# Performance work log

Hardware: AMD Instinct MI355X
Metric: run time of the kernel (lower is better)

Reference implementation:

```python
import jax, jax.numpy as jnp
import numpy as np

IFZ = 256      # in_features
SFZ = 1280     # sequence_features
AHZ = 8        # attention heads
AFZ = 64       # attention feature dim per head
NRES = 20      # canonical_num_residues
SCALE = float(np.sqrt(AFZ))
RESID = float(np.sqrt(2.0))
EPS = 1e-6


def _ln(x, s, b, eps=1e-5):
    m = jnp.mean(x, axis=-1, keepdims=True)
    v = jnp.var(x, axis=-1, keepdims=True)
    return (x - m) / jnp.sqrt(v + eps) * s + b


def setup_inputs() -> dict:
    key = jax.random.key(0)
    ks = jax.random.split(key, 20)
    N, B, S = 4096, 4, 512
    HD = AHZ * AFZ
    w = lambda k, shp: (jax.random.normal(k, shp, jnp.float32) * 0.02)
    d = {}
    d["x"] = jax.random.normal(ks[0], (N, IFZ), jnp.float32)
    d["packed_sequence_emb"] = jax.random.normal(ks[1], (B, S, SFZ), jnp.float32)
    d["packed_sequence_mask"] = jnp.ones((B, S), jnp.float32)
    d["prot_mask"] = jnp.arange(N, dtype=jnp.int32)
    d["batch"] = jax.random.randint(ks[2], (N,), 0, B, jnp.int32)
    # projections (bias=False)
    d["Wq"] = w(ks[3], (HD, IFZ))
    d["Wk"] = w(ks[4], (HD, SFZ))
    d["Wv"] = w(ks[5], (HD, SFZ))
    # ag: LayerNorm(HD) -> Linear(HD, IFZ, bias=False) (dropout = identity at eval)
    d["ag_ln_s"] = jnp.ones((HD,), jnp.float32)
    d["ag_ln_b"] = jnp.zeros((HD,), jnp.float32)
    d["Wag"] = w(ks[6], (IFZ, HD))
    d["res_ln_s"] = jnp.ones((3, IFZ), jnp.float32)
    d["res_ln_b"] = jnp.zeros((3, IFZ), jnp.float32)
    d["res_w1"] = w(ks[7], (3, IFZ, IFZ))
    d["res_b1"] = jnp.zeros((3, IFZ), jnp.float32)
    d["res_w2"] = w(ks[8], (3, IFZ, IFZ))
    d["res_b2"] = jnp.zeros((3, IFZ), jnp.float32)
    d["head_w"] = w(ks[9], (NRES, IFZ))
    d["head_b"] = jnp.zeros((NRES,), jnp.float32)
    # output LayerNorm en
    d["en_s"] = jnp.ones((IFZ,), jnp.float32)
    d["en_b"] = jnp.zeros((IFZ,), jnp.float32)
    return d


def _forward(x, emb, mask, prot_mask, batch, Wq, Wk, Wv, ag_ln_s, ag_ln_b, Wag,
             res_ln_s, res_ln_b, res_w1, res_b1, res_w2, res_b2,
             head_w, head_b, en_s, en_b):
    N = x.shape[0]
    B, S = emb.shape[:2]
    b_idx = batch[prot_mask]                      # [M]
    xp = x[prot_mask]                             # [M, IFZ]
    M = xp.shape[0]
    q = (xp @ Wq.T).reshape(M, AHZ, AFZ)          # [M,H,D]
    k = (emb @ Wk.T).reshape(B, S, AHZ, AFZ)      # [B,S,H,D]
    v = (emb @ Wv.T).reshape(B, S, AHZ, AFZ)
    # score vs every protein, then pick own protein (avoids materializing [M,S,H,D] gather)
    scores_all = jnp.einsum('mhd,bshd->mbsh', q, k) / SCALE          # [M,B,S,H]
    sel = b_idx[:, None, None, None]
    scores = jnp.take_along_axis(scores_all, sel, axis=1)[:, 0]       # [M,S,H]
    mb = mask[b_idx][:, :, None]                                      # [M,S,1]
    # padded_sequence_softmax: softmax over S, zero pads, renormalize
    sm = jax.nn.softmax(scores, axis=1) * mb
    w = sm / (jnp.sum(sm, axis=1, keepdims=True) + EPS)               # [M,S,H]
    feat_all = jnp.einsum('msh,bshd->mbhd', w, v)                     # [M,B,H,D]
    feat = jnp.take_along_axis(feat_all, sel, axis=1)[:, 0]
    feat = feat.reshape(M, AHZ * AFZ)
    ag = _ln(feat, ag_ln_s, ag_ln_b) @ Wag.T                          # [M, IFZ]
    # seq_aa_head on the scattered new features (identical to ag for unique prot_mask)
    h = ag
    for i in range(3):
        y = _ln(h, res_ln_s[i], res_ln_b[i])
        y = jax.nn.relu(y @ res_w1[i].T + res_b1[i])
        y = y @ res_w2[i].T + res_b2[i]
        h = (h + y) / RESID
    logits = h @ head_w.T + head_b                                     # [M, NRES]
    new_features = jnp.zeros_like(x).at[prot_mask].set(ag)
    seq_aa_logits = jnp.zeros((N, NRES), x.dtype).at[prot_mask].set(logits)
    unpacked_scores = jnp.zeros((N, S, AHZ), x.dtype).at[prot_mask].set(scores)
    out_x = _ln(x + new_features / RESID, en_s, en_b)
    return out_x, seq_aa_logits, unpacked_scores


def reference(x, packed_sequence_emb, packed_sequence_mask, prot_mask, batch,
              Wq, Wk, Wv, ag_ln_s, ag_ln_b, Wag,
              res_ln_s, res_ln_b, res_w1, res_b1, res_w2, res_b2,
              head_w, head_b, en_s, en_b):
    return _forward(x, packed_sequence_emb, packed_sequence_mask, prot_mask, batch,
                    Wq, Wk, Wv, ag_ln_s, ag_ln_b, Wag,
                    res_ln_s, res_ln_b, res_w1, res_b1, res_w2, res_b2,
                    head_w, head_b, en_s, en_b)
```

## Files before the change

kernel.cpp:

```cpp
#include <hip/hip_runtime.h>
#include <math.h>


typedef short bf8 __attribute__((ext_vector_type(8)));
typedef short bf4 __attribute__((ext_vector_type(4)));
typedef float f32x4 __attribute__((ext_vector_type(4)));
typedef unsigned short u16;

constexpr int LDT = 40;
#define RSQRT2 0.70710678118654752f

__device__ __forceinline__ u16 f2bf(float f) {
  unsigned int u = __builtin_bit_cast(unsigned int, f);
  unsigned int r = u + 0x7fffu + ((u >> 16) & 1u);
  return (u16)(r >> 16);
}
__device__ __forceinline__ float bf2f(u16 v) {
  return __builtin_bit_cast(float, (unsigned int)v << 16);
}
__device__ __forceinline__ f32x4 mfma16(bf8 a, bf8 b, f32x4 c) {
  return __builtin_amdgcn_mfma_f32_16x16x32_bf16(a, b, c, 0, 0, 0);
}

struct CvtDesc { const float* src; u16* dst; int n; };
struct CvtArgs { CvtDesc d[8]; int blk0[9]; };

__global__ __launch_bounds__(256) void cvt_k(
    CvtArgs a, const int* __restrict__ pm, const int* __restrict__ batch,
    int* __restrict__ list, int* __restrict__ inv, int* __restrict__ cnt,
    int N) {
  const int blk = blockIdx.x;
  if (blk >= a.blk0[8]) {
    int m = (blk - a.blk0[8]) * 256 + threadIdx.x;
    if (m >= N) return;
    int p = pm[m];
    int b = batch[p];
    int slot = atomicAdd(&cnt[b], 1);
    list[(size_t)b * N + slot] = m;
    inv[p] = m;
    return;
  }
  int d = 0;
#pragma unroll
  for (int k = 1; k < 8; ++k)
    if (blk >= a.blk0[k]) d = k;
  CvtDesc dd = a.d[d];
  int i = ((blk - a.blk0[d]) * 256 + threadIdx.x) * 8;
  if (i >= dd.n) return;
  f32x4 v0 = *(const f32x4*)(dd.src + i);
  f32x4 v1 = *(const f32x4*)(dd.src + i + 4);
  bf8 o;
  o[0] = (short)f2bf(v0[0]); o[1] = (short)f2bf(v0[1]);
  o[2] = (short)f2bf(v0[2]); o[3] = (short)f2bf(v0[3]);
  o[4] = (short)f2bf(v1[0]); o[5] = (short)f2bf(v1[1]);
  o[6] = (short)f2bf(v1[2]); o[7] = (short)f2bf(v1[3]);
  *(bf8*)(dd.dst + i) = o;
}

__global__ void init_idx_k(int* __restrict__ list, int* __restrict__ inv,
                           int* __restrict__ cnt, int N, int B) {
  int i = blockIdx.x * 256 + threadIdx.x;
  if (i < B * N) list[i] = -1;
  if (i < N) inv[i] = -1;
  if (i < B) cnt[i] = 0;
}

__device__ __forceinline__ void proj64_body(
    u16 (*As)[64 * LDT], u16 (*Bs)[64 * LDT],
    const u16* __restrict__ A, const u16* __restrict__ B,
    u16* __restrict__ C, int M, int Nn, int K, int lda, int ldb, int ldc,
    const int* __restrict__ gatherA, int m0, int n0, u16* __restrict__ VTout) {
  const int tid = threadIdx.x;
  const int wave = tid >> 6, lane = tid & 63;
  const int wm = (wave & 1) * 32, wn = (wave >> 1) * 32;
  const int lrow = lane & 15, quad = lane >> 4;
  const int srow = tid >> 2, skq = tid & 3;
  const bf8 z8 = {0, 0, 0, 0, 0, 0, 0, 0};
  const int off = srow * LDT + skq * 8;

  int gr0 = m0 + srow;
  int ar0 = (gr0 < M) ? (gatherA ? gatherA[gr0] : gr0) : -1;
  const u16* Ap0 = (ar0 >= 0) ? A + (size_t)ar0 * lda + skq * 8 : nullptr;
  const u16* Bp = (n0 + srow < Nn) ? B + (size_t)(n0 + srow) * ldb + skq * 8 : nullptr;

  {
    bf8 a0 = Ap0 ? *(const bf8*)Ap0 : z8;
    bf8 bv = Bp ? *(const bf8*)Bp : z8;
    *(bf8*)&As[0][off] = a0;
    *(bf8*)&Bs[0][off] = bv;
  }
  __syncthreads();

  f32x4 acc[2][2];
#pragma unroll
  for (int i = 0; i < 2; ++i)
#pragma unroll
    for (int j = 0; j < 2; ++j) acc[i][j] = (f32x4){0.f, 0.f, 0.f, 0.f};

  int cur = 0;
  for (int k0 = 0; k0 < K; k0 += 32) {
    const bool more = (k0 + 32 < K);
    bf8 na, nb;
    if (more) {
      na = Ap0 ? *(const bf8*)(Ap0 + k0 + 32) : z8;
      nb = Bp ? *(const bf8*)(Bp + k0 + 32) : z8;
    }
    bf8 af0 = *(const bf8*)&As[cur][(wm + lrow) * LDT + quad * 8];
    bf8 af1 = *(const bf8*)&As[cur][(wm + 16 + lrow) * LDT + quad * 8];
    bf8 bf0 = *(const bf8*)&Bs[cur][(wn + lrow) * LDT + quad * 8];
    bf8 bf1 = *(const bf8*)&Bs[cur][(wn + 16 + lrow) * LDT + quad * 8];
    acc[0][0] = mfma16(af0, bf0, acc[0][0]);
    acc[0][1] = mfma16(af0, bf1, acc[0][1]);
    acc[1][0] = mfma16(af1, bf0, acc[1][0]);
    acc[1][1] = mfma16(af1, bf1, acc[1][1]);
    if (more) {
      *(bf8*)&As[cur ^ 1][off] = na;
      *(bf8*)&Bs[cur ^ 1][off] = nb;
    }
    __syncthreads();
    cur ^= 1;
  }

#pragma unroll
  for (int i = 0; i < 2; ++i) {
    const int row0 = m0 + wm + i * 16 + quad * 4;
#pragma unroll
    for (int j = 0; j < 2; ++j) {
      int col = n0 + wn + j * 16 + lrow;
      if (col >= Nn) continue;
      if (VTout && col >= 512) {
        if (row0 < M) {
          int b = row0 >> 9, sl = row0 & 511;
          bf4 o;
#pragma unroll
          for (int r = 0; r < 4; ++r) o[r] = (short)f2bf(acc[i][j][r]);
          *(bf4*)&VTout[((size_t)(b * 512 + (col - 512)) * 512) + sl] = o;
        }
        continue;
      }
#pragma unroll
      for (int r = 0; r < 4; ++r) {
        int row = row0 + r;
        if (row >= M) continue;
        if (gatherA && gatherA[row] < 0) continue;
        C[(size_t)row * ldc + col] = f2bf(acc[i][j][r]);
      }
    }
  }
}

__global__ __launch_bounds__(256) void qkvproj_k(
    const u16* __restrict__ embbf, const u16* __restrict__ Wkvbf,
    u16* __restrict__ KVbf, u16* __restrict__ VT,
    const u16* __restrict__ xbf, const u16* __restrict__ Wqbf,
    u16* __restrict__ Qbf, const int* __restrict__ pm,
    int MKV, int N, int nkv) {
  __shared__ __align__(16) u16 As[2][64 * LDT];
  __shared__ __align__(16) u16 Bs[2][64 * LDT];
  const int blk = blockIdx.x;
  if (blk < nkv) {
    int by = blk >> 4, bx = blk & 15;
    proj64_body(As, Bs, embbf, Wkvbf, KVbf, MKV, 1024, 1280, 1280, 1280, 1024,
                nullptr, by * 64, bx * 64, VT);
  } else {
    int t = blk - nkv;
    int by = t >> 3, bx = t & 7;
    proj64_body(As, Bs, xbf, Wqbf, Qbf, N, 512, 256, 256, 256, 512,
                pm, by * 64, bx * 64, nullptr);
  }
}

constexpr int WST = 520;
constexpr int QST = 72;

__global__ __launch_bounds__(256) void attn_fused(
    const u16* __restrict__ Q, const u16* __restrict__ KV,
    const u16* __restrict__ VT, const int* __restrict__ list,
    const float* __restrict__ mask, u16* __restrict__ packed,
    u16* __restrict__ feat, int N) {
  const int NMT = gridDim.x;
  const int lin = blockIdx.y * NMT + blockIdx.x;
  const int xcd = lin & 7, rest = lin >> 3;
  const int mt = rest % NMT;
  const int y = ((rest / NMT) << 3) | xcd;
  const int b = y >> 3, h = y & 7;
  const int* lst = list + (size_t)b * N + mt * 32;
  if (lst[0] < 0) return;

  __shared__ __align__(16) u16 Ws[32 * WST];
  __shared__ __align__(16) u16 Qs[32 * QST];
  __shared__ __align__(16) u16 KVs[64 * QST];
  __shared__ __align__(16) float mk[8][68];
  __shared__ int mS[32];

  const int tid = threadIdx.x;
  const int wave = tid >> 6, lane = tid & 63;
  const int wm = (wave & 1) * 16, wns = (wave >> 1) * 32;
  const int lrow = lane & 15, quad = lane >> 4;
  const bf8 z8 = {0, 0, 0, 0, 0, 0, 0, 0};

  const int c0 = tid * 2, c1 = tid * 2 + 1;
  const int sr0 = c0 >> 3, kq0 = c0 & 7;
  const int sr1 = c1 >> 3, kq1 = c1 & 7;
  u16* kvw0 = &KVs[sr0 * QST + kq0 * 8];
  u16* kvw1 = &KVs[sr1 * QST + kq1 * 8];

  if (tid < 32) mS[tid] = lst[tid];
  {
    int p = tid >> 5, j = (tid & 31) * 2;
    *(float2*)&mk[p][j] = *(const float2*)&mask[(size_t)b * 512 + p * 64 + j];
  }
  {
    int qr = tid >> 3, kq = tid & 7;
    int m = lst[qr];
    *(bf8*)&Qs[qr * QST + kq * 8] =
        (m >= 0) ? *(const bf8*)(Q + (size_t)m * 512 + h * 64 + kq * 8) : z8;
  }
  const u16* KVb = KV + (size_t)(b * 512) * 1024 + h * 64;
  {
    int sta = mt & 7;
    *(bf8*)kvw0 = *(const bf8*)(KVb + (size_t)(sta * 64 + sr0) * 1024 + kq0 * 8);
    *(bf8*)kvw1 = *(const bf8*)(KVb + (size_t)(sta * 64 + sr1) * 1024 + kq1 * 8);
  }
  __syncthreads();

  const bf8 qa0 = *(const bf8*)&Qs[(wm + lrow) * QST + 0 + quad * 8];
  const bf8 qa1 = *(const bf8*)&Qs[(wm + lrow) * QST + 32 + quad * 8];

  bf8 r0, r1;
  for (int st = 0; st < 8; ++st) {
    const int sta = (st + mt) & 7;
    if (st < 7) {
      int nx = (st + 1 + mt) & 7;
      r0 = *(const bf8*)(KVb + (size_t)(nx * 64 + sr0) * 1024 + kq0 * 8);
      r1 = *(const bf8*)(KVb + (size_t)(nx * 64 + sr1) * 1024 + kq1 * 8);
    }
    f32x4 acc0 = {0.f, 0.f, 0.f, 0.f}, acc1 = acc0;
    {
      bf8 b00 = *(const bf8*)&KVs[(wns + lrow) * QST + quad * 8];
      bf8 b10 = *(const bf8*)&KVs[(wns + 16 + lrow) * QST + quad * 8];
      bf8 b01 = *(const bf8*)&KVs[(wns + lrow) * QST + 32 + quad * 8];
      bf8 b11 = *(const bf8*)&KVs[(wns + 16 + lrow) * QST + 32 + quad * 8];
      __builtin_amdgcn_s_setprio(1);
      acc0 = mfma16(qa0, b00, acc0);
      acc1 = mfma16(qa0, b10, acc1);
      acc0 = mfma16(qa1, b01, acc0);
      acc1 = mfma16(qa1, b11, acc1);
      __builtin_amdgcn_s_setprio(0);
    }
#pragma unroll
    for (int r = 0; r < 4; ++r) {
      int lr = wm + quad * 4 + r;
      Ws[lr * WST + sta * 64 + wns + lrow] = f2bf(acc0[r] * 0.125f);
      Ws[lr * WST + sta * 64 + wns + 16 + lrow] = f2bf(acc1[r] * 0.125f);
    }
    __syncthreads();
    if (st < 7) {
      *(bf8*)kvw0 = r0;
      *(bf8*)kvw1 = r1;
      __syncthreads();
    }
  }

  const u16* VTb = VT + (size_t)(b * 512 + h * 64) * 512;
  bf8 v0p = *(const bf8*)(VTb + (size_t)sr0 * 512 + ((mt & 7) << 6) + kq0 * 8);
  bf8 v1p = *(const bf8*)(VTb + (size_t)sr1 * 512 + ((mt & 7) << 6) + kq1 * 8);

  {
    const int row = tid >> 3, part = tid & 7;
    u16* wrow = &Ws[row * WST + part * 64];
    const int mm = mS[row];
    bf8 w[8];
    float mx = -1e30f;
#pragma unroll
    for (int v = 0; v < 8; ++v) {
      w[v] = *(const bf8*)(wrow + v * 8);
#pragma unroll
      for (int j = 0; j < 8; ++j) mx = fmaxf(mx, bf2f((u16)w[v][j]));
    }
    if (mm >= 0) {
      u16* prow = packed + ((size_t)h * N + mm) * 512 + part * 64;
#pragma unroll
      for (int v = 0; v < 8; ++v) *(bf8*)(prow + v * 8) = w[v];
    }
#pragma unroll
    for (int d = 1; d < 8; d <<= 1) mx = fmaxf(mx, __shfl_xor(mx, d));
    float ev[64];
    float se = 0.f, ms = 0.f;
#pragma unroll
    for (int v = 0; v < 8; ++v) {
      f32x4 m0 = *(const f32x4*)&mk[part][v * 8];
      f32x4 m1 = *(const f32x4*)&mk[part][v * 8 + 4];
#pragma unroll
      for (int j = 0; j < 8; ++j) {
        float e = __expf(bf2f((u16)w[v][j]) - mx);
        ev[v * 8 + j] = e;
        se += e;
        ms += e * (j < 4 ? m0[j] : m1[j - 4]);
      }
    }
#pragma unroll
    for (int d = 1; d < 8; d <<= 1) {
      se += __shfl_xor(se, d);
      ms += __shfl_xor(ms, d);
    }
    float iv = 1.0f / (ms + 1e-6f * se);
#pragma unroll
    for (int v = 0; v < 8; ++v) {
      f32x4 m0 = *(const f32x4*)&mk[part][v * 8];
      f32x4 m1 = *(const f32x4*)&mk[part][v * 8 + 4];
      bf8 o;
#pragma unroll
      for (int j = 0; j < 8; ++j)
        o[j] = (short)f2bf(ev[v * 8 + j] * (j < 4 ? m0[j] : m1[j - 4]) * iv);
      *(bf8*)(wrow + v * 8) = o;
    }
  }
  __syncthreads();
  *(bf8*)kvw0 = v0p;
  *(bf8*)kvw1 = v1p;
  __syncthreads();

  f32x4 acc0 = {0.f, 0.f, 0.f, 0.f}, acc1 = acc0;
  for (int ss = 0; ss < 8; ++ss) {
    const int s0 = ((ss + mt) & 7) << 6;
    if (ss < 7) {
      int nx = ((ss + 1 + mt) & 7) << 6;
      v0p = *(const bf8*)(VTb + (size_t)sr0 * 512 + nx + kq0 * 8);
      v1p = *(const bf8*)(VTb + (size_t)sr1 * 512 + nx + kq1 * 8);
    }
#pragma unroll
    for (int k0 = 0; k0 < 64; k0 += 32) {
      bf8 a = *(const bf8*)&Ws[(wm + lrow) * WST + s0 + k0 + quad * 8];
      bf8 b0 = *(const bf8*)&KVs[(wns + lrow) * QST + k0 + quad * 8];
      bf8 b1 = *(const bf8*)&KVs[(wns + 16 + lrow) * QST + k0 + quad * 8];
      __builtin_amdgcn_s_setprio(1);
      acc0 = mfma16(a, b0, acc0);
      acc1 = mfma16(a, b1, acc1);
      __builtin_amdgcn_s_setprio(0);
    }
    __syncthreads();
    if (ss < 7) {
      *(bf8*)kvw0 = v0p;
      *(bf8*)kvw1 = v1p;
      __syncthreads();
    }
  }
#pragma unroll
  for (int r = 0; r < 4; ++r) {
    int lr = wm + quad * 4 + r;
    int mm = mS[lr];
    if (mm < 0) continue;
    u16* frow = feat + (size_t)mm * 512 + h * 64;
    frow[wns + lrow] = f2bf(acc0[r]);
    frow[wns + 16 + lrow] = f2bf(acc1[r]);
  }
}

constexpr int HST = 268;
constexpr int AST = 520;
constexpr int YST = 280;
constexpr int SMEM_BYTES = 16 * HST * 4 + 16 * AST * 2 + 16 * YST * 2;

__global__ __launch_bounds__(1024) void mlp_unpack(
    const u16* __restrict__ feat, const float* __restrict__ ag_s,
    const float* __restrict__ ag_b, const u16* __restrict__ Wag,
    const float* __restrict__ x, const float* __restrict__ ens,
    const float* __restrict__ enb, const float* __restrict__ rls,
    const float* __restrict__ rlb, const u16* __restrict__ rw1,
    const float* __restrict__ rb1, const u16* __restrict__ rw2,
    const float* __restrict__ rb2, const float* __restrict__ hw,
    const float* __restrict__ hb, const int* __restrict__ pm,
    const u16* __restrict__ packed, float* __restrict__ out_sc,
    float* __restrict__ out_lg, float* __restrict__ out_x,
    int nmlp, int N) {
  __shared__ __align__(16) char smem[SMEM_BYTES];
  const int tid = threadIdx.x;

  if (blockIdx.x >= nmlp) {
    u16* Ls = (u16*)smem;
    const int g = tid >> 8, t = tid & 255;
    const int m = (blockIdx.x - nmlp) * 4 + g;
    u16* Lg = Ls + g * (8 * 520);
    int h = t >> 5, c = (t & 31) * 16;
    const u16* row = packed + ((size_t)h * N + m) * 512 + c;
    *(bf8*)&Lg[h * 520 + c] = *(const bf8*)row;
    *(bf8*)&Lg[h * 520 + c + 8] = *(const bf8*)(row + 8);
    __syncthreads();
    float* orow = out_sc + (size_t)pm[m] * 4096;
#pragma unroll
    for (int i = 0; i < 16; ++i) {
      int e = t + i * 256;
      orow[e] = bf2f(Lg[(e & 7) * 520 + (e >> 3)]);
    }
    return;
  }

  float* Hs = (float*)smem;
  u16* As = (u16*)(smem + 16 * HST * 4);
  u16* Ys = (u16*)(smem + 16 * HST * 4 + 16 * AST * 2);
  const int m0 = blockIdx.x * 16;
  const int wave = tid >> 6, lane = tid & 63;
  const int lrow = lane & 15, quad = lane >> 4;
  const int wn = wave * 16;
  const int row = wave;
  const int wq8 = quad * 8;
  const int nrow = pm[m0 + row];

  const u16* WagW = Wag + (size_t)(wn + lrow) * 512 + wq8;
  const u16* W1W = rw1 + (size_t)(wn + lrow) * 256 + wq8;
  const u16* W2W = rw2 + (size_t)(wn + lrow) * 256 + wq8;

  bf8 wp[8];
#pragma unroll
  for (int i = 0; i < 8; ++i) wp[i] = *(const bf8*)(WagW + i * 32);

  {
    const u16* frow = feat + (size_t)(m0 + row) * 512 + lane * 8;
    bf8 f0 = *(const bf8*)frow;
    float s = 0.f, sq = 0.f;
#pragma unroll
    for (int j = 0; j < 8; ++j) {
      float a = bf2f((u16)f0[j]);
      s += a;
      sq += a * a;
    }
#pragma unroll
    for (int d = 1; d < 64; d <<= 1) { s += __shfl_xor(s, d); sq += __shfl_xor(sq, d); }
    float mean = s * (1.0f / 512.0f);
    float var = sq * (1.0f / 512.0f) - mean * mean;
    float is = 1.0f / sqrtf(var + 1e-5f);
    int c = lane * 8;
    bf8 o0;
#pragma unroll
    for (int j = 0; j < 8; ++j)
      o0[j] = (short)f2bf((bf2f((u16)f0[j]) - mean) * is * ag_s[c + j] + ag_b[c + j]);
    *(bf8*)&As[row * AST + c] = o0;
  }
  __syncthreads();

  {
    f32x4 acc = {0.f, 0.f, 0.f, 0.f};
#pragma unroll
    for (int i = 0; i < 8; ++i) {
      bf8 a = *(const bf8*)&As[lrow * AST + i * 32 + wq8];
      acc = mfma16(a, wp[i], acc);
      wp[i] = *(const bf8*)(WagW + 256 + i * 32);
    }
#pragma unroll
    for (int i = 0; i < 8; ++i) {
      bf8 a = *(const bf8*)&As[lrow * AST + 256 + i * 32 + wq8];
      acc = mfma16(a, wp[i], acc);
      wp[i] = *(const bf8*)(W1W + i * 32);
    }
#pragma unroll
    for (int r = 0; r < 4; ++r) {
      int rr = quad * 4 + r;
      Hs[rr * HST + wn + lrow] = acc[r];
    }
  }
  __syncthreads();

  {
    int c = lane * 4;
    f32x4 xv = *(const f32x4*)&x[(size_t)nrow * 256 + c];
    f32x4 hv = *(const f32x4*)&Hs[row * HST + c];
    f32x4 v;
#pragma unroll
    for (int e = 0; e < 4; ++e) v[e] = xv[e] + hv[e] * RSQRT2;
    float s = v[0] + v[1] + v[2] + v[3];
    float sq = v[0] * v[0] + v[1] * v[1] + v[2] * v[2] + v[3] * v[3];
#pragma unroll
    for (int d = 1; d < 64; d <<= 1) { s += __shfl_xor(s, d); sq += __shfl_xor(sq, d); }
    float mean = s * (1.0f / 256.0f);
    float var = sq * (1.0f / 256.0f) - mean * mean;
    float is = 1.0f / sqrtf(var + 1e-5f);
    f32x4 o;
#pragma unroll
    for (int e = 0; e < 4; ++e)
      o[e] = (v[e] - mean) * is * ens[c + e] + enb[c + e];
    *(f32x4*)&out_x[(size_t)nrow * 256 + c] = o;
  }

  for (int layer = 0; layer < 3; ++layer) {
    {
      int c = lane * 4;
      f32x4 h0 = *(const f32x4*)&Hs[row * HST + c];
      float s = h0[0] + h0[1] + h0[2] + h0[3];
      float sq = h0[0] * h0[0] + h0[1] * h0[1] + h0[2] * h0[2] + h0[3] * h0[3];
#pragma unroll
      for (int d = 1; d < 64; d <<= 1) { s += __shfl_xor(s, d); sq += __shfl_xor(sq, d); }
      float mean = s * (1.0f / 256.0f);
      float var = sq * (1.0f / 256.0f) - mean * mean;
      float is = 1.0f / sqrtf(var + 1e-5f);
      const float* g = rls + layer * 256;
      const float* bb = rlb + layer * 256;
      bf4 o;
#pragma unroll
      for (int e = 0; e < 4; ++e)
        o[e] = (short)f2bf((h0[e] - mean) * is * g[c + e] + bb[c + e]);
      *(bf4*)&As[row * AST + c] = o;
    }
    __syncthreads();

    {
      f32x4 acc = {0.f, 0.f, 0.f, 0.f};
#pragma unroll
      for (int i = 0; i < 8; ++i) {
        bf8 a = *(const bf8*)&As[lrow * AST + i * 32 + wq8];
        acc = mfma16(a, wp[i], acc);
        wp[i] = *(const bf8*)(W2W + (size_t)layer * 65536 + i * 32);
      }
      float bi = rb1[layer * 256 + wn + lrow];
#pragma unroll
      for (int r = 0; r < 4; ++r) {
        int rr = quad * 4 + r;
        Ys[rr * YST + wn + lrow] = f2bf(fmaxf(acc[r] + bi, 0.f));
      }
    }
    __syncthreads();

    {
      f32x4 acc = {0.f, 0.f, 0.f, 0.f};
#pragma unroll
      for (int i = 0; i < 8; ++i) {
        bf8 a = *(const bf8*)&Ys[lrow * YST + i * 32 + wq8];
        acc = mfma16(a, wp[i], acc);
        if (layer < 2)
          wp[i] = *(const bf8*)(W1W + (size_t)(layer + 1) * 65536 + i * 32);
      }
      float bi = rb2[layer * 256 + wn + lrow];
#pragma unroll
      for (int r = 0; r < 4; ++r) {
        int rr = quad * 4 + r;
        float* h0 = &Hs[rr * HST + wn + lrow];
        *h0 = (*h0 + acc[r] + bi) * RSQRT2;
      }
    }
    __syncthreads();
  }

  if (lane < 20) {
    const float* hrow = &Hs[row * HST];
    const float* wrow = hw + (size_t)lane * 256;
    float l0 = 0.f, l1 = 0.f, l2 = 0.f, l3 = 0.f;
    for (int k = 0; k < 256; k += 16) {
      f32x4 h0 = *(const f32x4*)&hrow[k];
      f32x4 h1 = *(const f32x4*)&hrow[k + 4];
      f32x4 h2 = *(const f32x4*)&hrow[k + 8];
      f32x4 h3 = *(const f32x4*)&hrow[k + 12];
      f32x4 w0 = *(const f32x4*)&wrow[k];
      f32x4 w1 = *(const f32x4*)&wrow[k + 4];
      f32x4 w2 = *(const f32x4*)&wrow[k + 8];
      f32x4 w3 = *(const f32x4*)&wrow[k + 12];
#pragma unroll
      for (int e = 0; e < 4; ++e) {
        l0 += h0[e] * w0[e];
        l1 += h1[e] * w1[e];
        l2 += h2[e] * w2[e];
        l3 += h3[e] * w3[e];
      }
    }
    out_lg[(size_t)nrow * 20 + lane] = l0 + l1 + l2 + l3 + hb[lane];
  }
}

__global__ __launch_bounds__(256) void outx_k(
    const float* __restrict__ x, const int* __restrict__ inv,
    const float* __restrict__ g, const float* __restrict__ bb,
    float* __restrict__ out, int N) {
  __shared__ float red[256];
  int tid = threadIdx.x;
  for (int n = blockIdx.x; n < N; n += gridDim.x) {
    if (inv[n] >= 0) continue;
    __syncthreads();
    float v = x[(size_t)n * 256 + tid];
    red[tid] = v;
    __syncthreads();
    for (int off = 128; off; off >>= 1) {
      if (tid < off) red[tid] += red[tid + off];
      __syncthreads();
    }
    float mean = red[0] * (1.0f / 256.0f);
    __syncthreads();
    red[tid] = v * v;
    __syncthreads();
    for (int off = 128; off; off >>= 1) {
      if (tid < off) red[tid] += red[tid + off];
      __syncthreads();
    }
    float var = red[0] * (1.0f / 256.0f) - mean * mean;
    float is = 1.0f / sqrtf(var + 1e-5f);
    out[(size_t)n * 256 + tid] = (v - mean) * is * g[tid] + bb[tid];
    __syncthreads();
  }
}

extern "C" void kernel_launch(void* const* d_in, const int* in_sizes, int n_in,
                              void* d_out, int out_size, void* d_ws,
                              size_t ws_size, hipStream_t stream) {
  const float* x = (const float*)d_in[0];
  const float* emb = (const float*)d_in[1];
  const float* mask = (const float*)d_in[2];
  const int* pm = (const int*)d_in[3];
  const int* batch = (const int*)d_in[4];
  const float* Wq = (const float*)d_in[5];
  const float* Wk = (const float*)d_in[6];
  const float* Wv = (const float*)d_in[7];
  const float* ag_s = (const float*)d_in[8];
  const float* ag_b = (const float*)d_in[9];
  const float* Wag = (const float*)d_in[10];
  const float* rls = (const float*)d_in[11];
  const float* rlb = (const float*)d_in[12];
  const float* rw1 = (const float*)d_in[13];
  const float* rb1 = (const float*)d_in[14];
  const float* rw2 = (const float*)d_in[15];
  const float* rb2 = (const float*)d_in[16];
  const float* hw = (const float*)d_in[17];
  const float* hb = (const float*)d_in[18];
  const float* ens = (const float*)d_in[19];
  const float* enb = (const float*)d_in[20];

  const int N = in_sizes[0] / 256;
  const int B = in_sizes[2] / 512;

  char* wsb = (char*)d_ws;
  u16* embbf = (u16*)(wsb + 0);
  u16* xbf   = (u16*)(wsb + 5242880);
  u16* Wkvbf = (u16*)(wsb + 7340032);
  u16* Wqbf  = (u16*)(wsb + 9961472);
  u16* packed = (u16*)(wsb + 0);
  u16* KVbf   = (u16*)(wsb + 33554432);
  u16* Qbf    = (u16*)(wsb + 37748736);
  u16* VT     = (u16*)(wsb + 41943040);
  u16* featE  = (u16*)(wsb + 44040192);
  u16* Wagbf = (u16*)(wsb + 48234496);
  u16* rw1bf = (u16*)(wsb + 48496640);
  u16* rw2bf = (u16*)(wsb + 48889856);
  int* list  = (int*)(wsb + 49545216);
  int* inv   = (int*)(wsb + 49610752);
  int* cnt   = (int*)(wsb + 49627136);

  float* out_x = (float*)d_out;
  float* out_lg = out_x + (size_t)N * 256;
  float* out_sc = out_lg + (size_t)N * 20;

  init_idx_k<<<(B * N + 255) / 256, 256, 0, stream>>>(list, inv, cnt, N, B);
  CvtArgs ca;
  ca.d[0] = {emb, embbf, B * 512 * 1280};
  ca.d[1] = {x, xbf, 4096 * 256};
  ca.d[2] = {Wk, Wkvbf, 512 * 1280};
  ca.d[3] = {Wv, Wkvbf + 512 * 1280, 512 * 1280};
  ca.d[4] = {Wq, Wqbf, 512 * 256};
  ca.d[5] = {Wag, Wagbf, 256 * 512};
  ca.d[6] = {rw1, rw1bf, 3 * 256 * 256};
  ca.d[7] = {rw2, rw2bf, 3 * 256 * 256};
  {
    int acc = 0;
    for (int k = 0; k < 8; ++k) {
      ca.blk0[k] = acc;
      acc += (ca.d[k].n / 8 + 255) / 256;
    }
    ca.blk0[8] = acc;
    const int ncompact = (N + 255) / 256;
    cvt_k<<<acc + ncompact, 256, 0, stream>>>(ca, pm, batch, list, inv, cnt, N);
  }

  const int nkv = (B * 512 / 64) * 16;
  const int nq = (N / 64) * 8;
  qkvproj_k<<<nkv + nq, 256, 0, stream>>>(
      embbf, Wkvbf, KVbf, VT, xbf, Wqbf, Qbf, pm, B * 512, N, nkv);

  attn_fused<<<dim3(N / 32, B * 8), 256, 0, stream>>>(
      Qbf, KVbf, VT, list, mask, packed, featE, N);

  const int nmlp = N / 16;
  const int nunp = N / 4;
  mlp_unpack<<<dim3(nmlp + nunp), 1024, 0, stream>>>(
      featE, ag_s, ag_b, Wagbf, x, ens, enb, rls, rlb, rw1bf, rb1,
      rw2bf, rb2, hw, hb, pm, packed, out_sc, out_lg, out_x, nmlp, N);

  outx_k<<<64, 256, 0, stream>>>(x, inv, ens, enb, out_x, N);
}
```

Measured before the change: 280.7 us.

## Double K/V stage tile to 128 rows, load Q and mask directly from global

The attention kernel now stages 128 sequence rows of K (and of V^T) per iteration instead of 64, so each of the QK^T and PV loops runs 4 stages instead of 8 and needs half as many barriers. Each wave computes a wider 16x64 score tile. Q fragments are read straight from global into registers, and the softmax reads the mask straight from global, so the Qs and mask shared buffers are gone. In exchange each thread holds more prefetch registers, and the uncached mask reads in the softmax may add latency.

```diff
diff --git a/kernel.cpp b/kernel.cpp
--- a/kernel.cpp
+++ b/kernel.cpp
@@ -171,7 +171,8 @@
 }
 
 constexpr int WST = 520;
-constexpr int QST = 72;
+constexpr int KST = 72;
+constexpr int VST = 136;
 
 __global__ __launch_bounds__(256) void attn_fused(
     const u16* __restrict__ Q, const u16* __restrict__ KV,
@@ -188,88 +189,96 @@
   if (lst[0] < 0) return;
 
   __shared__ __align__(16) u16 Ws[32 * WST];
-  __shared__ __align__(16) u16 Qs[32 * QST];
-  __shared__ __align__(16) u16 KVs[64 * QST];
-  __shared__ __align__(16) float mk[8][68];
+  __shared__ __align__(16) u16 KVs[128 * KST];
   __shared__ int mS[32];
 
   const int tid = threadIdx.x;
   const int wave = tid >> 6, lane = tid & 63;
-  const int wm = (wave & 1) * 16, wns = (wave >> 1) * 32;
+  const int wm = (wave & 1) * 16;
+  const int wsn = (wave >> 1) * 64;
+  const int wnd = (wave >> 1) * 32;
   const int lrow = lane & 15, quad = lane >> 4;
   const bf8 z8 = {0, 0, 0, 0, 0, 0, 0, 0};
 
-  const int c0 = tid * 2, c1 = tid * 2 + 1;
-  const int sr0 = c0 >> 3, kq0 = c0 & 7;
-  const int sr1 = c1 >> 3, kq1 = c1 & 7;
-  u16* kvw0 = &KVs[sr0 * QST + kq0 * 8];
-  u16* kvw1 = &KVs[sr1 * QST + kq1 * 8];
+  const u16* KVb = KV + (size_t)(b * 512) * 1024 + h * 64;
+  const u16* VTb = VT + (size_t)(b * 512 + h * 64) * 512;
 
   if (tid < 32) mS[tid] = lst[tid];
   {
-    int p = tid >> 5, j = (tid & 31) * 2;
-    *(float2*)&mk[p][j] = *(const float2*)&mask[(size_t)b * 512 + p * 64 + j];
-  }
+    int sta = mt & 3;
+#pragma unroll
+    for (int i = 0; i < 4; ++i) {
+      int c = tid * 4 + i, sr = c >> 3, kq = c & 7;
+      *(bf8*)&KVs[sr * KST + kq * 8] =
+          *(const bf8*)(KVb + (size_t)(sta * 128 + sr) * 1024 + kq * 8);
+    }
+  }
+  __syncthreads();
+
+  const int qrow = mS[wm + lrow];
+  const u16* Qr = Q + (size_t)qrow * 512 + h * 64 + quad * 8;
+  const bf8 qa0 = (qrow >= 0) ? *(const bf8*)Qr : z8;
+  const bf8 qa1 = (qrow >= 0) ? *(const bf8*)(Qr + 32) : z8;
+
+  bf8 ra[4];
+  for (int st = 0; st < 4; ++st) {
+    const int sta = (st + mt) & 3;
+    if (st < 3) {
+      int nxt = (st + 1 + mt) & 3;
+#pragma unroll
+      for (int i = 0; i < 4; ++i) {
+        int c = tid * 4 + i, sr = c >> 3, kq = c & 7;
+        ra[i] = *(const bf8*)(KVb + (size_t)(nxt * 128 + sr) * 1024 + kq * 8);
+      }
+    }
+    f32x4 acc[4];
+#pragma unroll
+    for (int sf = 0; sf < 4; ++sf) acc[sf] = (f32x4){0.f, 0.f, 0.f, 0.f};
+    __builtin_amdgcn_s_setprio(1);
+#pragma unroll
+    for (int sf = 0; sf < 4; ++sf) {
+      int scol = wsn + sf * 16;
+      bf8 b0 = *(const bf8*)&KVs[(scol + lrow) * KST + quad * 8];
+      bf8 b1 = *(const bf8*)&KVs[(scol + lrow) * KST + 32 + quad * 8];
+      acc[sf] = mfma16(qa0, b0, acc[sf]);
+      acc[sf] = mfma16(qa1, b1, acc[sf]);
+    }
+    __builtin_amdgcn_s_setprio(0);
+#pragma unroll
+    for (int sf = 0; sf < 4; ++sf) {
+      int scol = wsn + sf * 16;
+#pragma unroll
+      for (int r = 0; r < 4; ++r) {
+        int lr = wm + quad * 4 + r;
+        Ws[lr * WST + (sta << 7) + scol + lrow] = f2bf(acc[sf][r] * 0.125f);
+      }
+    }
+    __syncthreads();
+    if (st < 3) {
+#pragma unroll
+      for (int i = 0; i < 4; ++i) {
+        int c = tid * 4 + i, sr = c >> 3, kq = c & 7;
+        *(bf8*)&KVs[sr * KST + kq * 8] = ra[i];
+      }
+      __syncthreads();
+    }
+  }
+
+  bf8 vp[4];
   {
-    int qr = tid >> 3, kq = tid & 7;
-    int m = lst[qr];
-    *(bf8*)&Qs[qr * QST + kq * 8] =
-        (m >= 0) ? *(const bf8*)(Q + (size_t)m * 512 + h * 64 + kq * 8) : z8;
-  }
-  const u16* KVb = KV + (size_t)(b * 512) * 1024 + h * 64;
-  {
-    int sta = mt & 7;
-    *(bf8*)kvw0 = *(const bf8*)(KVb + (size_t)(sta * 64 + sr0) * 1024 + kq0 * 8);
-    *(bf8*)kvw1 = *(const bf8*)(KVb + (size_t)(sta * 64 + sr1) * 1024 + kq1 * 8);
-  }
-  __syncthreads();
-
-  const bf8 qa0 = *(const bf8*)&Qs[(wm + lrow) * QST + 0 + quad * 8];
-  const bf8 qa1 = *(const bf8*)&Qs[(wm + lrow) * QST + 32 + quad * 8];
-
-  bf8 r0, r1;
-  for (int st = 0; st < 8; ++st) {
-    const int sta = (st + mt) & 7;
-    if (st < 7) {
-      int nx = (st + 1 + mt) & 7;
-      r0 = *(const bf8*)(KVb + (size_t)(nx * 64 + sr0) * 1024 + kq0 * 8);
-      r1 = *(const bf8*)(KVb + (size_t)(nx * 64 + sr1) * 1024 + kq1 * 8);
-    }
-    f32x4 acc0 = {0.f, 0.f, 0.f, 0.f}, acc1 = acc0;
-    {
-      bf8 b00 = *(const bf8*)&KVs[(wns + lrow) * QST + quad * 8];
-      bf8 b10 = *(const bf8*)&KVs[(wns + 16 + lrow) * QST + quad * 8];
-      bf8 b01 = *(const bf8*)&KVs[(wns + lrow) * QST + 32 + quad * 8];
-      bf8 b11 = *(const bf8*)&KVs[(wns + 16 + lrow) * QST + 32 + quad * 8];
-      __builtin_amdgcn_s_setprio(1);
-      acc0 = mfma16(qa0, b00, acc0);
-      acc1 = mfma16(qa0, b10, acc1);
-      acc0 = mfma16(qa1, b01, acc0);
-      acc1 = mfma16(qa1, b11, acc1);
-      __builtin_amdgcn_s_setprio(0);
-    }
-#pragma unroll
-    for (int r = 0; r < 4; ++r) {
-      int lr = wm + quad * 4 + r;
-      Ws[lr * WST + sta * 64 + wns + lrow] = f2bf(acc0[r] * 0.125f);
-      Ws[lr * WST + sta * 64 + wns + 16 + lrow] = f2bf(acc1[r] * 0.125f);
-    }
-    __syncthreads();
-    if (st < 7) {
-      *(bf8*)kvw0 = r0;
-      *(bf8*)kvw1 = r1;
-      __syncthreads();
-    }
-  }
-
-  const u16* VTb = VT + (size_t)(b * 512 + h * 64) * 512;
-  bf8 v0p = *(const bf8*)(VTb + (size_t)sr0 * 512 + ((mt & 7) << 6) + kq0 * 8);
-  bf8 v1p = *(const bf8*)(VTb + (size_t)sr1 * 512 + ((mt & 7) << 6) + kq1 * 8);
+    int s0 = (mt & 3) << 7;
+#pragma unroll
+    for (int i = 0; i < 4; ++i) {
+      int c = tid * 4 + i, vr = c >> 4, vq = c & 15;
+      vp[i] = *(const bf8*)(VTb + (size_t)vr * 512 + s0 + vq * 8);
+    }
+  }
 
   {
     const int row = tid >> 3, part = tid & 7;
     u16* wrow = &Ws[row * WST + part * 64];
     const int mm = mS[row];
+    const float* mkp = mask + (size_t)b * 512 + part * 64;
     bf8 w[8];
     float mx = -1e30f;
 #pragma unroll
@@ -289,8 +298,8 @@
     float se = 0.f, ms = 0.f;
 #pragma unroll
     for (int v = 0; v < 8; ++v) {
-      f32x4 m0 = *(const f32x4*)&mk[part][v * 8];
-      f32x4 m1 = *(const f32x4*)&mk[part][v * 8 + 4];
+      f32x4 m0 = *(const f32x4*)(mkp + v * 8);
+      f32x4 m1 = *(const f32x4*)(mkp + v * 8 + 4);
 #pragma unroll
       for (int j = 0; j < 8; ++j) {
         float e = __expf(bf2f((u16)w[v][j]) - mx);
@@ -307,8 +316,8 @@
     float iv = 1.0f / (ms + 1e-6f * se);
 #pragma unroll
     for (int v = 0; v < 8; ++v) {
-      f32x4 m0 = *(const f32x4*)&mk[part][v * 8];
-      f32x4 m1 = *(const f32x4*)&mk[part][v * 8 + 4];
+      f32x4 m0 = *(const f32x4*)(mkp + v * 8);
+      f32x4 m1 = *(const f32x4*)(mkp + v * 8 + 4);
       bf8 o;
 #pragma unroll
       for (int j = 0; j < 8; ++j)
@@ -317,32 +326,41 @@
     }
   }
   __syncthreads();
-  *(bf8*)kvw0 = v0p;
-  *(bf8*)kvw1 = v1p;
+#pragma unroll
+  for (int i = 0; i < 4; ++i) {
+    int c = tid * 4 + i, vr = c >> 4, vq = c & 15;
+    *(bf8*)&KVs[vr * VST + vq * 8] = vp[i];
+  }
   __syncthreads();
 
   f32x4 acc0 = {0.f, 0.f, 0.f, 0.f}, acc1 = acc0;
-  for (int ss = 0; ss < 8; ++ss) {
-    const int s0 = ((ss + mt) & 7) << 6;
-    if (ss < 7) {
-      int nx = ((ss + 1 + mt) & 7) << 6;
-      v0p = *(const bf8*)(VTb + (size_t)sr0 * 512 + nx + kq0 * 8);
-      v1p = *(const bf8*)(VTb + (size_t)sr1 * 512 + nx + kq1 * 8);
-    }
-#pragma unroll
-    for (int k0 = 0; k0 < 64; k0 += 32) {
-      bf8 a = *(const bf8*)&Ws[(wm + lrow) * WST + s0 + k0 + quad * 8];
-      bf8 b0 = *(const bf8*)&KVs[(wns + lrow) * QST + k0 + quad * 8];
-      bf8 b1 = *(const bf8*)&KVs[(wns + 16 + lrow) * QST + k0 + quad * 8];
-      __builtin_amdgcn_s_setprio(1);
+  for (int ss = 0; ss < 4; ++ss) {
+    const int s0 = ((ss + mt) & 3) << 7;
+    if (ss < 3) {
+      int nx = ((ss + 1 + mt) & 3) << 7;
+#pragma unroll
+      for (int i = 0; i < 4; ++i) {
+        int c = tid * 4 + i, vr = c >> 4, vq = c & 15;
+        vp[i] = *(const bf8*)(VTb + (size_t)vr * 512 + nx + vq * 8);
+      }
+    }
+    __builtin_amdgcn_s_setprio(1);
+#pragma unroll
+    for (int kk = 0; kk < 4; ++kk) {
+      bf8 a = *(const bf8*)&Ws[(wm + lrow) * WST + s0 + kk * 32 + quad * 8];
+      bf8 b0 = *(const bf8*)&KVs[(wnd + lrow) * VST + kk * 32 + quad * 8];
+      bf8 b1 = *(const bf8*)&KVs[(wnd + 16 + lrow) * VST + kk * 32 + quad * 8];
       acc0 = mfma16(a, b0, acc0);
       acc1 = mfma16(a, b1, acc1);
-      __builtin_amdgcn_s_setprio(0);
-    }
-    __syncthreads();
-    if (ss < 7) {
-      *(bf8*)kvw0 = v0p;
-      *(bf8*)kvw1 = v1p;
+    }
+    __builtin_amdgcn_s_setprio(0);
+    __syncthreads();
+    if (ss < 3) {
+#pragma unroll
+      for (int i = 0; i < 4; ++i) {
+        int c = tid * 4 + i, vr = c >> 4, vq = c & 15;
+        *(bf8*)&KVs[vr * VST + vq * 8] = vp[i];
+      }
       __syncthreads();
     }
   }
@@ -352,8 +370,8 @@
     int mm = mS[lr];
     if (mm < 0) continue;
     u16* frow = feat + (size_t)mm * 512 + h * 64;
-    frow[wns + lrow] = f2bf(acc0[r]);
-    frow[wns + 16 + lrow] = f2bf(acc1[r]);
+    frow[wnd + lrow] = f2bf(acc0[r]);
+    frow[wnd + 16 + lrow] = f2bf(acc1[r]);
   }
 }
 
```

Measured after the change: 285.1 us. No clear change (+1.6%).
